# Performance work log

Measured on AMD Instinct MI355X. Metric: run time of the kernel, lower is better.

Reference implementation:

```python
import jax, jax.numpy as jnp
import numpy as np

B, S, DIM, NUM_TYPES = 2048, 50, 128, 32000
EPS = 1e-5


def _l2norm(x):
    # torch F.normalize(p=2, dim=-1, eps=1e-5): x / max(||x||_2, eps)
    n = jnp.sqrt(jnp.sum(x * x, axis=-1, keepdims=True))
    return x / jnp.maximum(n, EPS)


def setup_inputs() -> dict:
    key = jax.random.key(0)
    ks = jax.random.split(key, 8)
    enc_output = jax.random.normal(ks[0], (B, S, DIM), dtype=jnp.float32)
    event_type = jax.random.randint(ks[1], (B, S), 0, NUM_TYPES, dtype=jnp.int64)
    user_type = jax.random.randint(ks[2], (B,), 0, NUM_TYPES, dtype=jnp.int64)
    # xavier_normal_ for [num_types, dim] weight: std = sqrt(2/(fan_in+fan_out))
    std = float(np.sqrt(2.0 / (DIM + NUM_TYPES)))
    W1 = jax.random.normal(ks[3], (NUM_TYPES, DIM), dtype=jnp.float32) * std
    W2 = jax.random.normal(ks[4], (NUM_TYPES, DIM), dtype=jnp.float32) * std
    W3 = jax.random.normal(ks[5], (NUM_TYPES, DIM), dtype=jnp.float32) * std
    W4 = jax.random.normal(ks[6], (NUM_TYPES, DIM), dtype=jnp.float32) * std
    one = jnp.ones((1,), dtype=jnp.float32)
    return {"enc_output": enc_output, "event_type": event_type, "user_type": user_type,
            "W1": W1, "W2": W2, "W3": W3, "W4": W4,
            "a": one, "b": one, "c": one, "d": one}


def reference(enc_output, event_type, user_type, W1, W2, W3, W4, a, b, c, d):
    # mean over time axis
    data = jnp.mean(enc_output, axis=1)  # [B, dim]
    p1 = _l2norm(jnp.einsum("bd,td->bt", data, W1))  # [B, num_types]
    p2 = _l2norm(jnp.einsum("bd,td->bt", data, W2))
    p3 = _l2norm(jnp.einsum("bd,td->bt", data, W3))
    p4 = _l2norm(jnp.einsum("bd,td->bt", data, W4))
    out = jnp.tanh(p1 * a + p2 * b + p3 * c + p4 * d)

    # Vectorized replacement of the per-sample python loop:
    # target_[i][e-1] = 0 for all nonzero events e; pad column absorbs zeros.
    bsz, num_types = out.shape[0], W1.shape[0]
    idx = jnp.where(event_type > 0, event_type - 1, num_types)  # [B, S]
    rows = jnp.arange(bsz)[:, None]
    target = jnp.ones((bsz, num_types + 1), dtype=out.dtype)
    target = target.at[rows, idx].set(0.0)
    target = target[:, :num_types]
    return out, target
```

## Files before the change

### kernel.cpp

```cpp
#include <hip/hip_runtime.h>
#include <stdint.h>

#define B_SZ 2048
#define S_SZ 50
#define D_SZ 128
#define T_SZ 32000

typedef __attribute__((ext_vector_type(8))) short short8v;
typedef __attribute__((ext_vector_type(4))) float floatx4;

__device__ __forceinline__ unsigned short f2bf(float f) {
  uint32_t u = __float_as_uint(f);
  uint32_t r = (u + 0x7fffu + ((u >> 16) & 1u)) >> 16;
  return (unsigned short)r;
}

__global__ __launch_bounds__(256) void k_mean(const float* __restrict__ enc,
                                              float* __restrict__ data) {
  int wid = threadIdx.x >> 6;
  int lane = threadIdx.x & 63;
  int b = blockIdx.x * 4 + wid;
  const float* src = enc + (size_t)b * (S_SZ * D_SZ) + lane * 2;
  float s0 = 0.f, s1 = 0.f;
#pragma unroll
  for (int s = 0; s < S_SZ; ++s) {
    float2 v = *(const float2*)(src + s * D_SZ);
    s0 += v.x; s1 += v.y;
  }
  float2 o; o.x = s0 * (1.f / 50.f); o.y = s1 * (1.f / 50.f);
  *(float2*)(data + (size_t)b * D_SZ + lane * 2) = o;
}

__global__ __launch_bounds__(256) void k_cast(const float* __restrict__ W1, const float* __restrict__ W2,
                                              const float* __restrict__ W3, const float* __restrict__ W4,
                                              unsigned short* __restrict__ w4) {
  int c = blockIdx.x * 256 + threadIdx.x;
  int e = c * 8;
  int t = e >> 9;
  int col = e & 511;
  int i = col >> 7;
  int d = col & 127;
  const float* src = (i == 0) ? W1 : (i == 1) ? W2 : (i == 2) ? W3 : W4;
  src += (size_t)t * 128 + d;
  float4 a = *(const float4*)src;
  float4 b = *(const float4*)(src + 4);
  union { short8v v; unsigned short u[8]; } pk;
  pk.u[0] = f2bf(a.x); pk.u[1] = f2bf(a.y); pk.u[2] = f2bf(a.z); pk.u[3] = f2bf(a.w);
  pk.u[4] = f2bf(b.x); pk.u[5] = f2bf(b.y); pk.u[6] = f2bf(b.z); pk.u[7] = f2bf(b.w);
  *(short8v*)(w4 + (size_t)t * 512 + col) = pk.v;
}

__global__ __launch_bounds__(256) void k_gram(const unsigned short* __restrict__ w4,
                                              float* __restrict__ Gp) {
  __shared__ unsigned short WT[128 * 72];
  int tid = threadIdx.x;
  int lane = tid & 63, wid = tid >> 6;
  int mat = blockIdx.x / 50;
  int chunk = blockIdx.x % 50;
  int t0 = chunk * 640;

  floatx4 acc[2][8];
#pragma unroll
  for (int aa = 0; aa < 2; ++aa)
#pragma unroll
    for (int n = 0; n < 8; ++n) acc[aa][n] = (floatx4){0.f, 0.f, 0.f, 0.f};

  for (int ks = 0; ks < 10; ++ks) {
    __syncthreads();
    const unsigned short* srow = w4 + (size_t)(t0 + ks * 64 + lane) * 512 + mat * 128;
#pragma unroll
    for (int r = 0; r < 4; ++r) {
      int ch = wid + r * 4;
      uint4 v = *(const uint4*)(srow + ch * 8);
      int dbase = ch * 8;
      WT[(dbase + 0) * 72 + lane] = (unsigned short)(v.x & 0xffff);
      WT[(dbase + 1) * 72 + lane] = (unsigned short)(v.x >> 16);
      WT[(dbase + 2) * 72 + lane] = (unsigned short)(v.y & 0xffff);
      WT[(dbase + 3) * 72 + lane] = (unsigned short)(v.y >> 16);
      WT[(dbase + 4) * 72 + lane] = (unsigned short)(v.z & 0xffff);
      WT[(dbase + 5) * 72 + lane] = (unsigned short)(v.z >> 16);
      WT[(dbase + 6) * 72 + lane] = (unsigned short)(v.w & 0xffff);
      WT[(dbase + 7) * 72 + lane] = (unsigned short)(v.w >> 16);
    }
    __syncthreads();
#pragma unroll
    for (int kk = 0; kk < 2; ++kk) {
      int kb = kk * 32 + (lane >> 4) * 8;
      short8v af[2], bfr[8];
#pragma unroll
      for (int aa = 0; aa < 2; ++aa) {
        int row = (wid * 2 + aa) * 16 + (lane & 15);
        af[aa] = *(const short8v*)&WT[row * 72 + kb];
      }
#pragma unroll
      for (int n = 0; n < 8; ++n) {
        int row = n * 16 + (lane & 15);
        bfr[n] = *(const short8v*)&WT[row * 72 + kb];
      }
#pragma unroll
      for (int aa = 0; aa < 2; ++aa)
#pragma unroll
        for (int n = 0; n < 8; ++n)
          acc[aa][n] = __builtin_amdgcn_mfma_f32_16x16x32_bf16(af[aa], bfr[n], acc[aa][n], 0, 0, 0);
    }
  }
  float* gp = Gp + (size_t)blockIdx.x * 16384;
  int g8 = lane >> 4, lc = lane & 15;
#pragma unroll
  for (int aa = 0; aa < 2; ++aa)
#pragma unroll
    for (int n = 0; n < 8; ++n)
#pragma unroll
      for (int q = 0; q < 4; ++q) {
        int row = (wid * 2 + aa) * 16 + g8 * 4 + q;
        int col = n * 16 + lc;
        gp[row * 128 + col] = acc[aa][n][q];
      }
}

__global__ __launch_bounds__(256) void k_greduce(const float* __restrict__ Gp,
                                                 float* __restrict__ G) {
  int mat = blockIdx.x >> 4;
  int e = ((blockIdx.x & 15) * 256 + threadIdx.x) * 4;
  const float* src = Gp + (size_t)(mat * 50) * 16384 + e;
  float4 s = {0.f, 0.f, 0.f, 0.f};
#pragma unroll 10
  for (int c = 0; c < 50; ++c) {
    float4 v = *(const float4*)(src + (size_t)c * 16384);
    s.x += v.x; s.y += v.y; s.z += v.z; s.w += v.w;
  }
  *(float4*)(G + (size_t)mat * 16384 + e) = s;
}

__global__ __launch_bounds__(256) void k_norm(const float* __restrict__ data, const float* __restrict__ G,
                                              const float* __restrict__ pa, const float* __restrict__ pb,
                                              const float* __restrict__ pc, const float* __restrict__ pd,
                                              unsigned short* __restrict__ data4) {
  __shared__ float dsh[16][132];
  __shared__ float Gch[32][132];
  __shared__ float sc[16][4];
  int tid = threadIdx.x;
  int b0 = blockIdx.x * 16;

  {
    int e = tid * 8;
    int rr = e >> 7, cc = e & 127;
    float4 v0 = *(const float4*)(data + (size_t)(b0 + rr) * 128 + cc);
    float4 v1 = *(const float4*)(data + (size_t)(b0 + rr) * 128 + cc + 4);
    *(float4*)&dsh[rr][cc] = v0;
    *(float4*)&dsh[rr][cc + 4] = v1;
  }
  int bl = tid >> 4, sub = tid & 15;
  float ss[4];
#pragma unroll
  for (int i = 0; i < 4; ++i) ss[i] = 0.f;

#pragma unroll
  for (int i = 0; i < 4; ++i) {
    for (int jc = 0; jc < 4; ++jc) {
      __syncthreads();
      {
        int e = tid * 16;
        int rr = e >> 7, cc = e & 127;
        const float* gsrc = G + i * 16384 + (jc * 32 + rr) * 128 + cc;
#pragma unroll
        for (int q = 0; q < 4; ++q)
          *(float4*)&Gch[rr][cc + q * 4] = *(const float4*)(gsrc + q * 4);
      }
      __syncthreads();
#pragma unroll
      for (int j2 = 0; j2 < 2; ++j2) {
        int jl = sub + j2 * 16;
        float tmp = 0.f;
#pragma unroll 8
        for (int k4 = 0; k4 < 32; ++k4) {
          float4 g = *(const float4*)&Gch[jl][k4 * 4];
          float4 dd = *(const float4*)&dsh[bl][k4 * 4];
          tmp += g.x * dd.x + g.y * dd.y + g.z * dd.z + g.w * dd.w;
        }
        ss[i] += dsh[bl][jc * 32 + jl] * tmp;
      }
    }
  }
#pragma unroll
  for (int i = 0; i < 4; ++i) {
    ss[i] += __shfl_xor(ss[i], 1);
    ss[i] += __shfl_xor(ss[i], 2);
    ss[i] += __shfl_xor(ss[i], 4);
    ss[i] += __shfl_xor(ss[i], 8);
  }
  if (sub == 0) {
    float cf0 = pa[0], cf1 = pb[0], cf2 = pc[0], cf3 = pd[0];
    sc[bl][0] = cf0 / fmaxf(sqrtf(ss[0]), 1e-5f);
    sc[bl][1] = cf1 / fmaxf(sqrtf(ss[1]), 1e-5f);
    sc[bl][2] = cf2 / fmaxf(sqrtf(ss[2]), 1e-5f);
    sc[bl][3] = cf3 / fmaxf(sqrtf(ss[3]), 1e-5f);
  }
  __syncthreads();
  for (int e = tid; e < 16 * 512; e += 256) {
    int r = e >> 9, col = e & 511;
    int i = col >> 7, d = col & 127;
    float v = dsh[r][d] * sc[r][i];
    data4[(size_t)(b0 + r) * 512 + col] = f2bf(v);
  }
}

__global__ __launch_bounds__(256, 3) void k_gemm(const unsigned short* __restrict__ data4,
                                                 const unsigned short* __restrict__ w4,
                                                 float* __restrict__ out) {
  __shared__ unsigned short As[128 * 64];
  __shared__ unsigned short Bs[128 * 64];
  int tid = threadIdx.x, lane = tid & 63, wid = tid >> 6;
  int bid = blockIdx.x;
  int sb = (bid & 7) * 500 + (bid >> 3);
  int tn = sb / 16, tm = sb % 16;
  int m0 = tm * 128, n0 = tn * 128;
  int srow = lane >> 3, slot = lane & 7;
  int wrr = (wid >> 1) * 64, wcc = (wid & 1) * 64;

  floatx4 acc[4][4];
#pragma unroll
  for (int m = 0; m < 4; ++m)
#pragma unroll
    for (int n = 0; n < 4; ++n) acc[m][n] = (floatx4){0.f, 0.f, 0.f, 0.f};

  const char* Abase = (const char*)data4;
  const char* Bbase = (const char*)w4;

  for (int kt = 0; kt < 8; ++kt) {
    if (kt) __syncthreads();
#pragma unroll
    for (int u = 0; u < 4; ++u) {
      int row = wid * 32 + u * 8 + srow;
      int sw = ((slot ^ (row & 7)) * 16);
      const char* ga = Abase + (size_t)(m0 + row) * 1024 + kt * 128 + sw;
      const char* gb = Bbase + (size_t)(n0 + row) * 1024 + kt * 128 + sw;
      int lbo = __builtin_amdgcn_readfirstlane(wid * 4096 + u * 1024);
      __builtin_amdgcn_global_load_lds((const __attribute__((address_space(1))) void*)ga,
                                       (__attribute__((address_space(3))) void*)((char*)As + lbo), 16, 0, 0);
      __builtin_amdgcn_global_load_lds((const __attribute__((address_space(1))) void*)gb,
                                       (__attribute__((address_space(3))) void*)((char*)Bs + lbo), 16, 0, 0);
    }
    __syncthreads();
    int g8 = lane >> 4;
#pragma unroll
    for (int kk = 0; kk < 2; ++kk) {
      short8v af[4], bfr[4];
#pragma unroll
      for (int m = 0; m < 4; ++m) {
        int r = wrr + m * 16 + (lane & 15);
        int byteoff = r * 128 + (((kk * 4 + g8) ^ (r & 7)) * 16);
        af[m] = *(const short8v*)((const char*)As + byteoff);
      }
#pragma unroll
      for (int n = 0; n < 4; ++n) {
        int r = wcc + n * 16 + (lane & 15);
        int byteoff = r * 128 + (((kk * 4 + g8) ^ (r & 7)) * 16);
        bfr[n] = *(const short8v*)((const char*)Bs + byteoff);
      }
#pragma unroll
      for (int m = 0; m < 4; ++m)
#pragma unroll
        for (int n = 0; n < 4; ++n)
          acc[m][n] = __builtin_amdgcn_mfma_f32_16x16x32_bf16(af[m], bfr[n], acc[m][n], 0, 0, 0);
    }
  }
  int g8 = lane >> 4, lc = lane & 15;
#pragma unroll
  for (int m = 0; m < 4; ++m)
#pragma unroll
    for (int n = 0; n < 4; ++n)
#pragma unroll
      for (int q = 0; q < 4; ++q) {
        int row = m0 + wrr + m * 16 + g8 * 4 + q;
        int col = n0 + wcc + n * 16 + lc;
        float x = acc[m][n][q];
        float e2 = __expf(2.f * x);
        out[(size_t)row * 32000 + col] = (e2 - 1.f) / (e2 + 1.f);
      }
}

__global__ __launch_bounds__(256) void k_fill(const int* __restrict__ ev,
                                              float* __restrict__ target) {
  int b = blockIdx.x;
  float4* row4 = (float4*)(target + (size_t)b * 32000);
  float4 one = {1.f, 1.f, 1.f, 1.f};
#pragma unroll 4
  for (int j = threadIdx.x; j < 8000; j += 256) row4[j] = one;
  __syncthreads();
  if (threadIdx.x < 50) {
    int et = ev[b * 50 + threadIdx.x];
    if (et > 0) ((float*)row4)[et - 1] = 0.f;
  }
}

extern "C" void kernel_launch(void* const* d_in, const int* in_sizes, int n_in,
                              void* d_out, int out_size, void* d_ws, size_t ws_size,
                              hipStream_t stream) {
  const float* enc = (const float*)d_in[0];
  const int* ev = (const int*)d_in[1];
  const float* W1 = (const float*)d_in[3];
  const float* W2 = (const float*)d_in[4];
  const float* W3 = (const float*)d_in[5];
  const float* W4 = (const float*)d_in[6];
  const float* pa = (const float*)d_in[7];
  const float* pb = (const float*)d_in[8];
  const float* pc = (const float*)d_in[9];
  const float* pd = (const float*)d_in[10];

  float* out = (float*)d_out;
  float* target = out + (size_t)B_SZ * T_SZ;

  char* ws = (char*)d_ws;
  float* data = (float*)ws;
  unsigned short* data4 = (unsigned short*)(ws + (1 << 20));
  float* G = (float*)(ws + 3 * (1 << 20));
  unsigned short* w4 = (unsigned short*)(ws + 4 * (1 << 20));
  float* Gp = (float*)(ws + 36 * (size_t)(1 << 20));

  k_mean<<<512, 256, 0, stream>>>(enc, data);
  k_cast<<<8000, 256, 0, stream>>>(W1, W2, W3, W4, w4);
  k_gram<<<200, 256, 0, stream>>>(w4, Gp);
  k_greduce<<<64, 256, 0, stream>>>(Gp, G);
  k_norm<<<128, 256, 0, stream>>>(data, G, pa, pb, pc, pd, data4);
  k_gemm<<<4000, 256, 0, stream>>>(data4, w4, out);
  k_fill<<<2048, 256, 0, stream>>>(ev, target);
}
```

Before: 738.4 us.

## Fuse time-mean into norm kernel and double-buffer GEMM LDS tiles

The separate mean kernel is removed and the mean over the sequence axis is now computed inside the normalization kernel, which drops one launch and the round trip through an intermediate buffer. The GEMM now uses two LDS buffers, issuing the next K-tile's global-to-LDS loads before computing on the current tile, with explicit vmcnt waits and raw barriers. Occupancy is lowered from 3 to 2 blocks per CU because LDS use doubles. The mean now runs on only 128 blocks, so that part has less parallelism, and the GEMM is probably bound by its output writes, which limits what the overlap can hide.

Measured after the change: 734.8 us. No clear change (-0.5%).

```diff
diff --git a/kernel.cpp b/kernel.cpp
--- a/kernel.cpp
+++ b/kernel.cpp
@@ -13,22 +13,6 @@
   uint32_t u = __float_as_uint(f);
   uint32_t r = (u + 0x7fffu + ((u >> 16) & 1u)) >> 16;
   return (unsigned short)r;
-}
-
-__global__ __launch_bounds__(256) void k_mean(const float* __restrict__ enc,
-                                              float* __restrict__ data) {
-  int wid = threadIdx.x >> 6;
-  int lane = threadIdx.x & 63;
-  int b = blockIdx.x * 4 + wid;
-  const float* src = enc + (size_t)b * (S_SZ * D_SZ) + lane * 2;
-  float s0 = 0.f, s1 = 0.f;
-#pragma unroll
-  for (int s = 0; s < S_SZ; ++s) {
-    float2 v = *(const float2*)(src + s * D_SZ);
-    s0 += v.x; s1 += v.y;
-  }
-  float2 o; o.x = s0 * (1.f / 50.f); o.y = s1 * (1.f / 50.f);
-  *(float2*)(data + (size_t)b * D_SZ + lane * 2) = o;
 }
 
 __global__ __launch_bounds__(256) void k_cast(const float* __restrict__ W1, const float* __restrict__ W2,
@@ -132,7 +116,7 @@
   *(float4*)(G + (size_t)mat * 16384 + e) = s;
 }
 
-__global__ __launch_bounds__(256) void k_norm(const float* __restrict__ data, const float* __restrict__ G,
+__global__ __launch_bounds__(256) void k_norm(const float* __restrict__ enc, const float* __restrict__ G,
                                               const float* __restrict__ pa, const float* __restrict__ pb,
                                               const float* __restrict__ pc, const float* __restrict__ pd,
                                               unsigned short* __restrict__ data4) {
@@ -143,12 +127,22 @@
   int b0 = blockIdx.x * 16;
 
   {
-    int e = tid * 8;
-    int rr = e >> 7, cc = e & 127;
-    float4 v0 = *(const float4*)(data + (size_t)(b0 + rr) * 128 + cc);
-    float4 v1 = *(const float4*)(data + (size_t)(b0 + rr) * 128 + cc + 4);
-    *(float4*)&dsh[rr][cc] = v0;
-    *(float4*)&dsh[rr][cc + 4] = v1;
+    int r = tid >> 4;
+    int c8 = (tid & 15) * 8;
+    const float* src = enc + (size_t)(b0 + r) * (S_SZ * D_SZ) + c8;
+    float4 s0 = {0.f, 0.f, 0.f, 0.f}, s1 = {0.f, 0.f, 0.f, 0.f};
+#pragma unroll 10
+    for (int s = 0; s < S_SZ; ++s) {
+      float4 v0 = *(const float4*)(src + s * D_SZ);
+      float4 v1 = *(const float4*)(src + s * D_SZ + 4);
+      s0.x += v0.x; s0.y += v0.y; s0.z += v0.z; s0.w += v0.w;
+      s1.x += v1.x; s1.y += v1.y; s1.z += v1.z; s1.w += v1.w;
+    }
+    const float inv = 1.f / 50.f;
+    s0.x *= inv; s0.y *= inv; s0.z *= inv; s0.w *= inv;
+    s1.x *= inv; s1.y *= inv; s1.z *= inv; s1.w *= inv;
+    *(float4*)&dsh[r][c8] = s0;
+    *(float4*)&dsh[r][c8 + 4] = s1;
   }
   int bl = tid >> 4, sub = tid & 15;
   float ss[4];
@@ -205,11 +199,11 @@
   }
 }
 
-__global__ __launch_bounds__(256, 3) void k_gemm(const unsigned short* __restrict__ data4,
+__global__ __launch_bounds__(256, 2) void k_gemm(const unsigned short* __restrict__ data4,
                                                  const unsigned short* __restrict__ w4,
                                                  float* __restrict__ out) {
-  __shared__ unsigned short As[128 * 64];
-  __shared__ unsigned short Bs[128 * 64];
+  __shared__ unsigned short As[2][8192];
+  __shared__ unsigned short Bs[2][8192];
   int tid = threadIdx.x, lane = tid & 63, wid = tid >> 6;
   int bid = blockIdx.x;
   int sb = (bid & 7) * 500 + (bid >> 3);
@@ -227,35 +221,48 @@
   const char* Abase = (const char*)data4;
   const char* Bbase = (const char*)w4;
 
+#define STAGE(b, kt)                                                                        \
+  {                                                                                         \
+    _Pragma("unroll")                                                                       \
+    for (int u = 0; u < 4; ++u) {                                                           \
+      int row = wid * 32 + u * 8 + srow;                                                    \
+      int sw = ((slot ^ (row & 7)) * 16);                                                   \
+      const char* ga = Abase + (size_t)(m0 + row) * 1024 + (kt) * 128 + sw;                 \
+      const char* gb = Bbase + (size_t)(n0 + row) * 1024 + (kt) * 128 + sw;                 \
+      int lbo = __builtin_amdgcn_readfirstlane((b) * 16384 + wid * 4096 + u * 1024);        \
+      __builtin_amdgcn_global_load_lds((const __attribute__((address_space(1))) void*)ga,   \
+                                       (__attribute__((address_space(3))) void*)((char*)As + lbo), 16, 0, 0); \
+      __builtin_amdgcn_global_load_lds((const __attribute__((address_space(1))) void*)gb,   \
+                                       (__attribute__((address_space(3))) void*)((char*)Bs + lbo), 16, 0, 0); \
+    }                                                                                       \
+  }
+
+  STAGE(0, 0);
+
   for (int kt = 0; kt < 8; ++kt) {
-    if (kt) __syncthreads();
-#pragma unroll
-    for (int u = 0; u < 4; ++u) {
-      int row = wid * 32 + u * 8 + srow;
-      int sw = ((slot ^ (row & 7)) * 16);
-      const char* ga = Abase + (size_t)(m0 + row) * 1024 + kt * 128 + sw;
-      const char* gb = Bbase + (size_t)(n0 + row) * 1024 + kt * 128 + sw;
-      int lbo = __builtin_amdgcn_readfirstlane(wid * 4096 + u * 1024);
-      __builtin_amdgcn_global_load_lds((const __attribute__((address_space(1))) void*)ga,
-                                       (__attribute__((address_space(3))) void*)((char*)As + lbo), 16, 0, 0);
-      __builtin_amdgcn_global_load_lds((const __attribute__((address_space(1))) void*)gb,
-                                       (__attribute__((address_space(3))) void*)((char*)Bs + lbo), 16, 0, 0);
-    }
-    __syncthreads();
+    int cur = kt & 1;
+    if (kt < 7) {
+      STAGE(cur ^ 1, kt + 1);
+      asm volatile("s_waitcnt vmcnt(8)" ::: "memory");
+    } else {
+      asm volatile("s_waitcnt vmcnt(0)" ::: "memory");
+    }
+    __builtin_amdgcn_s_barrier();
     int g8 = lane >> 4;
+    int bb = cur * 16384;
 #pragma unroll
     for (int kk = 0; kk < 2; ++kk) {
       short8v af[4], bfr[4];
 #pragma unroll
       for (int m = 0; m < 4; ++m) {
         int r = wrr + m * 16 + (lane & 15);
-        int byteoff = r * 128 + (((kk * 4 + g8) ^ (r & 7)) * 16);
+        int byteoff = bb + r * 128 + (((kk * 4 + g8) ^ (r & 7)) * 16);
         af[m] = *(const short8v*)((const char*)As + byteoff);
       }
 #pragma unroll
       for (int n = 0; n < 4; ++n) {
         int r = wcc + n * 16 + (lane & 15);
-        int byteoff = r * 128 + (((kk * 4 + g8) ^ (r & 7)) * 16);
+        int byteoff = bb + r * 128 + (((kk * 4 + g8) ^ (r & 7)) * 16);
         bfr[n] = *(const short8v*)((const char*)Bs + byteoff);
       }
 #pragma unroll
@@ -264,7 +271,10 @@
         for (int n = 0; n < 4; ++n)
           acc[m][n] = __builtin_amdgcn_mfma_f32_16x16x32_bf16(af[m], bfr[n], acc[m][n], 0, 0, 0);
     }
-  }
+    __builtin_amdgcn_s_barrier();
+  }
+#undef STAGE
+
   int g8 = lane >> 4, lc = lane & 15;
 #pragma unroll
   for (int m = 0; m < 4; ++m)
@@ -312,17 +322,15 @@
   float* target = out + (size_t)B_SZ * T_SZ;
 
   char* ws = (char*)d_ws;
-  float* data = (float*)ws;
   unsigned short* data4 = (unsigned short*)(ws + (1 << 20));
   float* G = (float*)(ws + 3 * (1 << 20));
   unsigned short* w4 = (unsigned short*)(ws + 4 * (1 << 20));
   float* Gp = (float*)(ws + 36 * (size_t)(1 << 20));
 
-  k_mean<<<512, 256, 0, stream>>>(enc, data);
   k_cast<<<8000, 256, 0, stream>>>(W1, W2, W3, W4, w4);
   k_gram<<<200, 256, 0, stream>>>(w4, Gp);
   k_greduce<<<64, 256, 0, stream>>>(Gp, G);
-  k_norm<<<128, 256, 0, stream>>>(data, G, pa, pb, pc, pd, data4);
+  k_norm<<<128, 256, 0, stream>>>(enc, G, pa, pb, pc, pd, data4);
   k_gemm<<<4000, 256, 0, stream>>>(data4, w4, out);
   k_fill<<<2048, 256, 0, stream>>>(ev, target);
 }
```
